# Kernel tuning notes

Measured on AMD Instinct MI355X. Metric: run time of the kernel, lower is better.

## Reference

```python
import jax, jax.numpy as jnp
import numpy as np
from jax import lax

B, T, D, H = 32, 2048, 128, 256

def _lstm_dir(x, w_ih, w_hh, b_ih, b_hh, h0, c0, reverse):
    # x: (B,T,Din). Precompute input contributions for all timesteps.
    xw = jnp.einsum('btd,gd->tbg', x, w_ih) + (b_ih + b_hh)  # (T,B,4H)
    def step(carry, xt):
        h, c = carry
        g = xt + h @ w_hh.T                      # (B,4H), gate order i,f,g,o
        i, f, gg, o = jnp.split(g, 4, axis=-1)
        c = jax.nn.sigmoid(f) * c + jax.nn.sigmoid(i) * jnp.tanh(gg)
        h = jax.nn.sigmoid(o) * jnp.tanh(c)
        return (h, c), h
    (hn, cn), hs = lax.scan(step, (h0, c0), xw, reverse=reverse)
    return hs.transpose(1, 0, 2), hn, cn          # (B,T,H), (B,H), (B,H)

def _bilstm(x, pf, pr, h0f, c0f, h0r, c0r):
    of, hnf, cnf = _lstm_dir(x, *pf, h0f, c0f, False)
    orv, hnr, cnr = _lstm_dir(x, *pr, h0r, c0r, True)
    return jnp.concatenate([of, orv], axis=-1), hnf, cnf, hnr, cnr

def setup_inputs() -> dict:
    key = jax.random.key(0)
    ks = jax.random.split(key, 20)
    s = 0.05
    d = {'x': jax.random.normal(ks[0], (B, T, D), jnp.float32)}
    def mk(k, shape):
        return jax.random.normal(k, shape, jnp.float32) * s
    # layer 1 (input D), forward and reverse directions
    d['w_ih1_f'] = mk(ks[1], (4*H, D)); d['w_hh1_f'] = mk(ks[2], (4*H, H))
    d['b_ih1_f'] = mk(ks[3], (4*H,));  d['b_hh1_f'] = mk(ks[4], (4*H,))
    d['w_ih1_r'] = mk(ks[5], (4*H, D)); d['w_hh1_r'] = mk(ks[6], (4*H, H))
    d['b_ih1_r'] = mk(ks[7], (4*H,));  d['b_hh1_r'] = mk(ks[8], (4*H,))
    # layer 2 (input 2H)
    d['w_ih2_f'] = mk(ks[9], (4*H, 2*H)); d['w_hh2_f'] = mk(ks[10], (4*H, H))
    d['b_ih2_f'] = mk(ks[11], (4*H,));   d['b_hh2_f'] = mk(ks[12], (4*H,))
    d['w_ih2_r'] = mk(ks[13], (4*H, 2*H)); d['w_hh2_r'] = mk(ks[14], (4*H, H))
    d['b_ih2_r'] = mk(ks[15], (4*H,));    d['b_hh2_r'] = mk(ks[16], (4*H,))
    d['fc_w'] = mk(ks[17], (1, 2*H)); d['fc_b'] = mk(ks[18], (1,))
    return d

def reference(x, w_ih1_f, w_hh1_f, b_ih1_f, b_hh1_f,
              w_ih1_r, w_hh1_r, b_ih1_r, b_hh1_r,
              w_ih2_f, w_hh2_f, b_ih2_f, b_hh2_f,
              w_ih2_r, w_hh2_r, b_ih2_r, b_hh2_r,
              fc_w, fc_b):
    z = jnp.zeros((x.shape[0], H), x.dtype)
    # layer 1, zero initial state
    out1, hnf, cnf, hnr, cnr = _bilstm(
        x, (w_ih1_f, w_hh1_f, b_ih1_f, b_hh1_f),
        (w_ih1_r, w_hh1_r, b_ih1_r, b_hh1_r), z, z, z, z)
    # layer 2 initialized with layer 1 final (h,c) per direction (as in the
    # original: lstm2(lstm_out, lstm_c))
    out2, _, _, _, _ = _bilstm(
        out1, (w_ih2_f, w_hh2_f, b_ih2_f, b_hh2_f),
        (w_ih2_r, w_hh2_r, b_ih2_r, b_hh2_r), hnf, cnf, hnr, cnr)
    y = jnp.tanh(out2 @ fc_w.T + fc_b)            # (B,T,1)
    return y.reshape(y.shape[0], -1)[:, None, :]  # (B,1,T)
```

## Files before the change

kernel.cpp:

```cpp
#include <hip/hip_runtime.h>

#define BB 32
#define TT 2048
#define DD 128
#define HH 256
#define NTH 256
#define NRANK 32
#define NGRP 8
#define HASHK 2654435761u

typedef float f32x4 __attribute__((ext_vector_type(4)));
typedef unsigned int u32;
typedef u32 u32x2 __attribute__((ext_vector_type(2)));
typedef u32 u32x4 __attribute__((ext_vector_type(4)));

__device__ __forceinline__ float sigm(float x)  { return 1.0f / (1.0f + __expf(-x)); }
__device__ __forceinline__ float tanh_f(float x){ return 1.0f - 2.0f / (__expf(2.0f * x) + 1.0f); }

template<int KIN, int LAYER>
__global__ __launch_bounds__(NTH, 1)
void lstm_scan(const float* __restrict__ in_seq, long sb, long st,
               const float* __restrict__ wih_f, const float* __restrict__ whh_f,
               const float* __restrict__ bih_f, const float* __restrict__ bhh_f,
               const float* __restrict__ wih_r, const float* __restrict__ whh_r,
               const float* __restrict__ bih_r, const float* __restrict__ bhh_r,
               float* __restrict__ hseed,
               float* __restrict__ cseed,
               u32* __restrict__ hbt,
               float* __restrict__ out1,
               float* __restrict__ acc,
               const float* __restrict__ fcw,
               int never)
{
    constexpr int KZ   = KIN + HH;
    constexpr int KINP = KIN + 4;
    constexpr int HHP  = HH + 4;
    constexpr int C4   = KIN / 4;
    constexpr int XC   = KIN / 128;
    constexpr int NPX  = (8 * C4) / NTH;
    constexpr int RSTR = 36;
    constexpr int PADN = (LAYER == 1) ? 8192 : 5120;

    const int blk  = blockIdx.x;
    const int g    = blk & 7;
    const int rank = blk >> 3;
    const int dir  = g & 1;
    const int bq   = g >> 1;
    const int tid  = threadIdx.x;

    __shared__ __align__(16) float zx[8][KINP];
    __shared__ __align__(16) float zh[8][HHP];
    __shared__ __align__(16) float red2[256 * RSTR];
    __shared__ float gates_s[4][8][9];
    __shared__ float bias_s[32];
    __shared__ float padlds[PADN];
    if (never) padlds[never & (PADN - 1)] = 1.0f;

    const float* wih = dir ? wih_r : wih_f;
    const float* whh = dir ? whh_r : whh_f;
    const float* bih = dir ? bih_r : bih_f;
    const float* bhh = dir ? bhh_r : bhh_f;

    const int rg = tid >> 5;
    const int sl = tid & 31;

    f32x4 wx[4][XC], wh[4][2];
    #pragma unroll
    for (int rr = 0; rr < 4; ++rr) {
        const int r = rg * 4 + rr;
        const int grow = (r >> 3) * HH + rank * 8 + (r & 7);
        #pragma unroll
        for (int c = 0; c < XC; ++c)
            wx[rr][c] = *(const f32x4*)(wih + (long)grow * KIN + sl * 4 + 128 * c);
        #pragma unroll
        for (int c = 0; c < 2; ++c)
            wh[rr][c] = *(const f32x4*)(whh + (long)grow * HH + sl * 4 + 128 * c);
    }
    if (tid < 32) {
        const int grow = (tid >> 3) * HH + rank * 8 + (tid & 7);
        bias_s[tid] = bih[grow] + bhh[grow];
    }

    u32* hbt_g = hbt + g * (2 * 256 * 8 * 2);
    float* hs_seed = hseed + g * (8 * HH);
    float* cs_seed = cseed + g * (8 * HH);

    const int jj2   = tid >> 3;
    const int bl2   = tid & 7;
    const int jglob = rank * 8 + jj2;

    float creg = 0.0f, fcv = 0.0f;
    if (tid < 64 && LAYER == 2) {
        creg = cs_seed[bl2 * HH + jglob];
        fcv  = fcw[dir * HH + jglob];
    }

    {
        const int t0 = dir ? (TT - 1) : 0;
        const long tb = (long)t0 * st;
        for (int q = tid; q < 8 * C4; q += NTH) {
            const int bl = q / C4;
            const int k4 = q - bl * C4;
            *(f32x4*)&zx[bl][k4 * 4] =
                *(const f32x4*)(in_seq + (long)(bq * 8 + bl) * sb + tb + k4 * 4);
        }
        if (tid < 64) {
            const float h0 = (LAYER == 1) ? 0.0f : hs_seed[bl2 * HH + jglob];
            const u32 hx = __float_as_uint(h0);
            u32x2 pkt; pkt.x = hx; pkt.y = 1u + hx * HASHK;
            u32* pp = hbt_g + ((0 * 256 + jglob) * 8 + bl2) * 2;
            asm volatile("global_store_dwordx2 %0, %1, off sc0 sc1"
                         :: "v"(pp), "v"(pkt) : "memory");
        }
    }
    __syncthreads();

    for (int s = 0; s < TT; ++s) {
        const int t = dir ? (TT - 1 - s) : s;

        f32x4 px[NPX];
        if (s + 1 < TT) {
            const long tb = (long)(dir ? (t - 1) : (t + 1)) * st;
            #pragma unroll
            for (int i = 0; i < NPX; ++i) {
                const int q  = tid + i * NTH;
                const int bl = q / C4;
                const int k4 = q - bl * C4;
                px[i] = *(const f32x4*)(in_seq + (long)(bq * 8 + bl) * sb + tb + k4 * 4);
            }
        }

        float ac[4][8];
        #pragma unroll
        for (int rr = 0; rr < 4; ++rr)
            #pragma unroll
            for (int b = 0; b < 8; ++b) ac[rr][b] = 0.0f;
        #pragma unroll
        for (int c = 0; c < XC; ++c) {
            f32x4 zv[8];
            #pragma unroll
            for (int b = 0; b < 8; ++b)
                zv[b] = *(const f32x4*)&zx[b][sl * 4 + 128 * c];
            #pragma unroll
            for (int rr = 0; rr < 4; ++rr) {
                const f32x4 w = wx[rr][c];
                #pragma unroll
                for (int b = 0; b < 8; ++b)
                    ac[rr][b] = fmaf(w.x, zv[b].x, fmaf(w.y, zv[b].y,
                                fmaf(w.z, zv[b].z, fmaf(w.w, zv[b].w, ac[rr][b]))));
            }
        }

        {
            const u32 tg = (u32)(s + 1);
            const u32* hp = hbt_g + (((s & 1) * 256 + tid) * 8) * 2;
            u32x4 q0, q1, q2, q3;
            while (true) {
                asm volatile(
                    "global_load_dwordx4 %0, %4, off sc0 sc1\n\t"
                    "global_load_dwordx4 %1, %4, off offset:16 sc0 sc1\n\t"
                    "global_load_dwordx4 %2, %4, off offset:32 sc0 sc1\n\t"
                    "global_load_dwordx4 %3, %4, off offset:48 sc0 sc1\n\t"
                    "s_waitcnt vmcnt(0)"
                    : "=&v"(q0), "=&v"(q1), "=&v"(q2), "=&v"(q3)
                    : "v"(hp) : "memory");
                const bool ok =
                    (q0.y - q0.x * HASHK == tg) && (q0.w - q0.z * HASHK == tg) &&
                    (q1.y - q1.x * HASHK == tg) && (q1.w - q1.z * HASHK == tg) &&
                    (q2.y - q2.x * HASHK == tg) && (q2.w - q2.z * HASHK == tg) &&
                    (q3.y - q3.x * HASHK == tg) && (q3.w - q3.z * HASHK == tg);
                if (ok) break;
                __builtin_amdgcn_s_sleep(1);
            }
            zh[0][tid] = __uint_as_float(q0.x);
            zh[1][tid] = __uint_as_float(q0.z);
            zh[2][tid] = __uint_as_float(q1.x);
            zh[3][tid] = __uint_as_float(q1.z);
            zh[4][tid] = __uint_as_float(q2.x);
            zh[5][tid] = __uint_as_float(q2.z);
            zh[6][tid] = __uint_as_float(q3.x);
            zh[7][tid] = __uint_as_float(q3.z);
        }
        __syncthreads();

        #pragma unroll
        for (int c = 0; c < 2; ++c) {
            f32x4 zv[8];
            #pragma unroll
            for (int b = 0; b < 8; ++b)
                zv[b] = *(const f32x4*)&zh[b][sl * 4 + 128 * c];
            #pragma unroll
            for (int rr = 0; rr < 4; ++rr) {
                const f32x4 w = wh[rr][c];
                #pragma unroll
                for (int b = 0; b < 8; ++b)
                    ac[rr][b] = fmaf(w.x, zv[b].x, fmaf(w.y, zv[b].y,
                                fmaf(w.z, zv[b].z, fmaf(w.w, zv[b].w, ac[rr][b]))));
            }
        }
        #pragma unroll
        for (int rr = 0; rr < 4; ++rr)
            #pragma unroll
            for (int b = 0; b < 8; ++b)
                red2[((rg * 4 + rr) * 8 + b) * RSTR + sl] = ac[rr][b];
        __syncthreads();

        {
            float sg = bias_s[tid >> 3];
            const f32x4* rp = (const f32x4*)&red2[tid * RSTR];
            #pragma unroll
            for (int q = 0; q < 8; ++q) {
                const f32x4 v = rp[q];
                sg += v.x + v.y + v.z + v.w;
            }
            gates_s[tid >> 6][(tid >> 3) & 7][tid & 7] = sg;
        }
        __syncthreads();

        if (tid < 64) {
            const float gi = gates_s[0][jj2][bl2];
            const float gf = gates_s[1][jj2][bl2];
            const float gg = gates_s[2][jj2][bl2];
            const float go = gates_s[3][jj2][bl2];
            creg = sigm(gf) * creg + sigm(gi) * tanh_f(gg);
            const float hv = sigm(go) * tanh_f(creg);
            if (s + 1 < TT) {
                const u32 hx = __float_as_uint(hv);
                u32x2 pkt; pkt.x = hx; pkt.y = (u32)(s + 2) + hx * HASHK;
                u32* pp = hbt_g + ((((s + 1) & 1) * 256 + jglob) * 8 + bl2) * 2;
                asm volatile("global_store_dwordx2 %0, %1, off sc0 sc1"
                             :: "v"(pp), "v"(pkt) : "memory");
            }
            if (LAYER == 1) {
                out1[(long)t * (BB * 2 * HH) + (bq * 8 + bl2) * (2 * HH) + dir * HH + jglob] = hv;
                if (s == TT - 1) {
                    hs_seed[bl2 * HH + jglob] = hv;
                    cs_seed[bl2 * HH + jglob] = creg;
                }
            } else {
                float val = hv * fcv;
                val += __shfl_down(val, 32, 64);
                val += __shfl_down(val, 16, 64);
                val += __shfl_down(val, 8, 64);
                if (jj2 == 0) atomicAdd(&acc[t * BB + bq * 8 + bl2], val);
            }
        }
        if (s + 1 < TT) {
            #pragma unroll
            for (int i = 0; i < NPX; ++i) {
                const int q  = tid + i * NTH;
                const int bl = q / C4;
                const int k4 = q - bl * C4;
                *(f32x4*)&zx[bl][k4 * 4] = px[i];
            }
        }
        __syncthreads();
    }
}

__global__ void finalize_k(const float* __restrict__ acc, const float* __restrict__ fcb,
                           float* __restrict__ out)
{
    const int i = blockIdx.x * blockDim.x + threadIdx.x;
    if (i < BB * TT) {
        const int b = i >> 11;
        const int t = i & (TT - 1);
        out[i] = tanhf(acc[t * BB + b] + fcb[0]);
    }
}

extern "C" void kernel_launch(void* const* d_in, const int* in_sizes, int n_in,
                              void* d_out, int out_size, void* d_ws, size_t ws_size,
                              hipStream_t stream) {
    const float* x     = (const float*)d_in[0];
    const float* wih1f = (const float*)d_in[1];
    const float* whh1f = (const float*)d_in[2];
    const float* bih1f = (const float*)d_in[3];
    const float* bhh1f = (const float*)d_in[4];
    const float* wih1r = (const float*)d_in[5];
    const float* whh1r = (const float*)d_in[6];
    const float* bih1r = (const float*)d_in[7];
    const float* bhh1r = (const float*)d_in[8];
    const float* wih2f = (const float*)d_in[9];
    const float* whh2f = (const float*)d_in[10];
    const float* bih2f = (const float*)d_in[11];
    const float* bhh2f = (const float*)d_in[12];
    const float* wih2r = (const float*)d_in[13];
    const float* whh2r = (const float*)d_in[14];
    const float* bih2r = (const float*)d_in[15];
    const float* bhh2r = (const float*)d_in[16];
    const float* fcw   = (const float*)d_in[17];
    const float* fcb   = (const float*)d_in[18];

    char* ws = (char*)d_ws;
    size_t off = 0;
    float* acc  = (float*)(ws + off); off += (size_t)TT * BB * 4;
    u32* hbt1   = (u32*)(ws + off);   off += (size_t)NGRP * 2 * 256 * 8 * 2 * 4;
    u32* hbt2   = (u32*)(ws + off);   off += (size_t)NGRP * 2 * 256 * 8 * 2 * 4;
    float* hseed = (float*)(ws + off); off += (size_t)NGRP * 8 * HH * 4;
    float* cseed = (float*)(ws + off); off += (size_t)NGRP * 8 * HH * 4;
    const size_t clear_bytes = off;
    float* out1 = (float*)(ws + off); off += (size_t)TT * BB * 2 * HH * 4;

    hipMemsetAsync(d_ws, 0, clear_bytes, stream);

    lstm_scan<DD, 1><<<NGRP * NRANK, NTH, 0, stream>>>(
        x, (long)TT * DD, (long)DD,
        wih1f, whh1f, bih1f, bhh1f, wih1r, whh1r, bih1r, bhh1r,
        hseed, cseed, hbt1, out1, nullptr, nullptr, 0);

    lstm_scan<2 * HH, 2><<<NGRP * NRANK, NTH, 0, stream>>>(
        out1, (long)(2 * HH), (long)(BB * 2 * HH),
        wih2f, whh2f, bih2f, bhh2f, wih2r, whh2r, bih2r, bhh2r,
        hseed, cseed, hbt2, nullptr, acc, fcw, 0);

    finalize_k<<<(BB * TT + 255) / 256, 256, 0, stream>>>(acc, fcb, (float*)d_out);
}
```

Baseline: 12.80 ms.

## Probe XCC co-location to poll hidden state via L2 and issue polls early

At kernel start, each group of 32 blocks runs a handshake that reads the hardware XCC id and checks whether a stored magic value is visible through L2-coherent (sc0-only) loads. If every block in the group sits on the same XCC, the per-step spin-wait on the hidden-state exchange uses cheaper sc0 loads instead of system-coherent sc0 sc1 loads. It falls back to the coherent path after 512 failed polls. The first poll is now issued before the input-projection FMAs so its latency overlaps that compute, and the next-step input prefetch moves after the wait. This adds startup handshake cost and a hang or correctness risk if the same-XCC assumption breaks.

```diff
diff --git a/kernel.cpp b/kernel.cpp
--- a/kernel.cpp
+++ b/kernel.cpp
@@ -16,6 +16,29 @@
 
 __device__ __forceinline__ float sigm(float x)  { return 1.0f / (1.0f + __expf(-x)); }
 __device__ __forceinline__ float tanh_f(float x){ return 1.0f - 2.0f / (__expf(2.0f * x) + 1.0f); }
+
+__device__ __forceinline__ u32 ld_u32_ic(const u32* p) {
+    u32 v;
+    asm volatile("global_load_dword %0, %1, off sc0 sc1\n\ts_waitcnt vmcnt(0)"
+                 : "=v"(v) : "v"(p) : "memory");
+    return v;
+}
+__device__ __forceinline__ u32 ld_u32_l2(const u32* p) {
+    u32 v;
+    asm volatile("global_load_dword %0, %1, off sc0\n\ts_waitcnt vmcnt(0)"
+                 : "=v"(v) : "v"(p) : "memory");
+    return v;
+}
+__device__ __forceinline__ void st_u32_ic(u32* p, u32 v) {
+    asm volatile("global_store_dword %0, %1, off sc0 sc1" :: "v"(p), "v"(v) : "memory");
+}
+
+#define SPIN4(SC) asm volatile( \
+    "global_load_dwordx4 %0, %4, off " SC "\n\t" \
+    "global_load_dwordx4 %1, %4, off offset:16 " SC "\n\t" \
+    "global_load_dwordx4 %2, %4, off offset:32 " SC "\n\t" \
+    "global_load_dwordx4 %3, %4, off offset:48 " SC "\n\t" \
+    : "=&v"(q0), "=&v"(q1), "=&v"(q2), "=&v"(q3) : "v"(hp) : "memory")
 
 template<int KIN, int LAYER>
 __global__ __launch_bounds__(NTH, 1)
@@ -30,9 +53,9 @@
                float* __restrict__ out1,
                float* __restrict__ acc,
                const float* __restrict__ fcw,
+               u32* __restrict__ syncb,
                int never)
 {
-    constexpr int KZ   = KIN + HH;
     constexpr int KINP = KIN + 4;
     constexpr int HHP  = HH + 4;
     constexpr int C4   = KIN / 4;
@@ -53,6 +76,7 @@
     __shared__ __align__(16) float red2[256 * RSTR];
     __shared__ float gates_s[4][8][9];
     __shared__ float bias_s[32];
+    __shared__ u32 shb;
     __shared__ float padlds[PADN];
     if (never) padlds[never & (PADN - 1)] = 1.0f;
 
@@ -94,6 +118,49 @@
         creg = cs_seed[bl2 * HH + jglob];
         fcv  = fcw[dir * HH + jglob];
     }
+
+    bool fast;
+    {
+        const u32 MAGIC = 0xA5F00D01u;
+        const u32 xcc = __builtin_amdgcn_s_getreg((31u << 11) | 20u);
+        u32* pa = syncb +         (size_t)g * NRANK * 32;
+        u32* va = syncb +  8192 + (size_t)g * NRANK * 32;
+        u32* vb = syncb + 16384 + (size_t)g * NRANK * 32;
+        if (tid < 32) (void)ld_u32_l2(pa + tid * 32);
+        __syncthreads();
+        if (tid == 0) st_u32_ic(va + rank * 32, 1u);
+        if (tid < 32) {
+            u32 v;
+            do { v = ld_u32_ic(va + tid * 32);
+                 if (!v) __builtin_amdgcn_s_sleep(2); } while (!v);
+        }
+        __syncthreads();
+        if (tid == 0) st_u32_ic(pa + rank * 32, MAGIC);
+        bool ok = true;
+        if (tid < 32) {
+            u32 v = 0;
+            for (int it = 0; it < 1000; ++it) {
+                v = ld_u32_l2(pa + tid * 32);
+                if (v == MAGIC) break;
+                __builtin_amdgcn_s_sleep(1);
+            }
+            ok = (v == MAGIC);
+        }
+        ok = __all(ok);
+        if (tid == 0) st_u32_ic(vb + rank * 32, 1u | (ok ? 2u : 0u) | (xcc << 4));
+        bool okv = true;
+        if (tid < 32) {
+            u32 v;
+            do { v = ld_u32_ic(vb + tid * 32);
+                 if (!v) __builtin_amdgcn_s_sleep(2); } while (!v);
+            okv = ((v & 2u) != 0u) && ((v >> 4) == xcc);
+        }
+        okv = __all(okv);
+        if (tid == 0) shb = okv ? 1u : 0u;
+        __syncthreads();
+        fast = (shb != 0u);
+    }
+    bool use_l2 = fast;
 
     {
         const int t0 = dir ? (TT - 1) : 0;
@@ -118,17 +185,10 @@
     for (int s = 0; s < TT; ++s) {
         const int t = dir ? (TT - 1 - s) : s;
 
-        f32x4 px[NPX];
-        if (s + 1 < TT) {
-            const long tb = (long)(dir ? (t - 1) : (t + 1)) * st;
-            #pragma unroll
-            for (int i = 0; i < NPX; ++i) {
-                const int q  = tid + i * NTH;
-                const int bl = q / C4;
-                const int k4 = q - bl * C4;
-                px[i] = *(const f32x4*)(in_seq + (long)(bq * 8 + bl) * sb + tb + k4 * 4);
-            }
-        }
+        const u32 tg = (u32)(s + 1);
+        const u32* hp = hbt_g + (((s & 1) * 256 + tid) * 8) * 2;
+        u32x4 q0, q1, q2, q3;
+        if (use_l2) SPIN4("sc0"); else SPIN4("sc0 sc1");
 
         float ac[4][8];
         #pragma unroll
@@ -152,35 +212,41 @@
         }
 
         {
-            const u32 tg = (u32)(s + 1);
-            const u32* hp = hbt_g + (((s & 1) * 256 + tid) * 8) * 2;
-            u32x4 q0, q1, q2, q3;
+            int fails = 0;
             while (true) {
-                asm volatile(
-                    "global_load_dwordx4 %0, %4, off sc0 sc1\n\t"
-                    "global_load_dwordx4 %1, %4, off offset:16 sc0 sc1\n\t"
-                    "global_load_dwordx4 %2, %4, off offset:32 sc0 sc1\n\t"
-                    "global_load_dwordx4 %3, %4, off offset:48 sc0 sc1\n\t"
-                    "s_waitcnt vmcnt(0)"
-                    : "=&v"(q0), "=&v"(q1), "=&v"(q2), "=&v"(q3)
-                    : "v"(hp) : "memory");
-                const bool ok =
+                asm volatile("s_waitcnt vmcnt(0)" ::: "memory");
+                const bool okt =
                     (q0.y - q0.x * HASHK == tg) && (q0.w - q0.z * HASHK == tg) &&
                     (q1.y - q1.x * HASHK == tg) && (q1.w - q1.z * HASHK == tg) &&
                     (q2.y - q2.x * HASHK == tg) && (q2.w - q2.z * HASHK == tg) &&
                     (q3.y - q3.x * HASHK == tg) && (q3.w - q3.z * HASHK == tg);
-                if (ok) break;
-                __builtin_amdgcn_s_sleep(1);
-            }
-            zh[0][tid] = __uint_as_float(q0.x);
-            zh[1][tid] = __uint_as_float(q0.z);
-            zh[2][tid] = __uint_as_float(q1.x);
-            zh[3][tid] = __uint_as_float(q1.z);
-            zh[4][tid] = __uint_as_float(q2.x);
-            zh[5][tid] = __uint_as_float(q2.z);
-            zh[6][tid] = __uint_as_float(q3.x);
-            zh[7][tid] = __uint_as_float(q3.z);
-        }
+                if (okt) break;
+                if (use_l2) { if (++fails >= 512) use_l2 = false; }
+                else __builtin_amdgcn_s_sleep(1);
+                if (use_l2) SPIN4("sc0"); else SPIN4("sc0 sc1");
+            }
+        }
+
+        f32x4 px[NPX];
+        if (s + 1 < TT) {
+            const long tb = (long)(dir ? (t - 1) : (t + 1)) * st;
+            #pragma unroll
+            for (int i = 0; i < NPX; ++i) {
+                const int q  = tid + i * NTH;
+                const int bl = q / C4;
+                const int k4 = q - bl * C4;
+                px[i] = *(const f32x4*)(in_seq + (long)(bq * 8 + bl) * sb + tb + k4 * 4);
+            }
+        }
+
+        zh[0][tid] = __uint_as_float(q0.x);
+        zh[1][tid] = __uint_as_float(q0.z);
+        zh[2][tid] = __uint_as_float(q1.x);
+        zh[3][tid] = __uint_as_float(q1.z);
+        zh[4][tid] = __uint_as_float(q2.x);
+        zh[5][tid] = __uint_as_float(q2.z);
+        zh[6][tid] = __uint_as_float(q3.x);
+        zh[7][tid] = __uint_as_float(q3.z);
         __syncthreads();
 
         #pragma unroll
@@ -297,6 +363,8 @@
     float* acc  = (float*)(ws + off); off += (size_t)TT * BB * 4;
     u32* hbt1   = (u32*)(ws + off);   off += (size_t)NGRP * 2 * 256 * 8 * 2 * 4;
     u32* hbt2   = (u32*)(ws + off);   off += (size_t)NGRP * 2 * 256 * 8 * 2 * 4;
+    u32* sync1  = (u32*)(ws + off);   off += (size_t)3 * 8192 * 4;
+    u32* sync2  = (u32*)(ws + off);   off += (size_t)3 * 8192 * 4;
     float* hseed = (float*)(ws + off); off += (size_t)NGRP * 8 * HH * 4;
     float* cseed = (float*)(ws + off); off += (size_t)NGRP * 8 * HH * 4;
     const size_t clear_bytes = off;
@@ -307,12 +375,12 @@
     lstm_scan<DD, 1><<<NGRP * NRANK, NTH, 0, stream>>>(
         x, (long)TT * DD, (long)DD,
         wih1f, whh1f, bih1f, bhh1f, wih1r, whh1r, bih1r, bhh1r,
-        hseed, cseed, hbt1, out1, nullptr, nullptr, 0);
+        hseed, cseed, hbt1, out1, nullptr, nullptr, sync1, 0);
 
     lstm_scan<2 * HH, 2><<<NGRP * NRANK, NTH, 0, stream>>>(
         out1, (long)(2 * HH), (long)(BB * 2 * HH),
         wih2f, whh2f, bih2f, bhh2f, wih2r, whh2r, bih2r, bhh2r,
-        hseed, cseed, hbt2, nullptr, acc, fcw, 0);
+        hseed, cseed, hbt2, nullptr, acc, fcw, sync2, 0);
 
     finalize_k<<<(BB * TT + 255) / 256, 256, 0, stream>>>(acc, fcb, (float*)d_out);
 }
```

Result: slower. 14.66 ms (+14.5%).
